# Optimization experiments

Measured on AMD Instinct MI355X. Metric: run time of the kernel, lower is better.

## Reference

```python
import jax, jax.numpy as jnp
import numpy as np

B, S, D, H = 2, 2048, 2048, 16
HD = D // H


def setup_inputs() -> dict:
    key = jax.random.key(0)
    kx, = jax.random.split(key, 1)
    return {
        "x": jax.random.normal(kx, (B, S, D), dtype=jnp.float32),
        "q_mask": jnp.ones((D, D), dtype=jnp.float32),
        "k_mask": jnp.ones((D, D), dtype=jnp.float32),
        "v_mask": jnp.ones((D, D), dtype=jnp.float32),
        "out_mask": jnp.ones((D, D), dtype=jnp.float32),
        "head_mask": jnp.ones((H,), dtype=jnp.float32),
        "attention_mask": jnp.ones((B, S), dtype=jnp.float32),
        "shared_weight": jnp.float32(1.0),
    }


def reference(x, q_mask, k_mask, v_mask, out_mask, head_mask, attention_mask, shared_weight):
    b, s, d = x.shape
    scale = jnp.float32(HD) ** -0.5

    def shared_linear(inp, mask):
        # F.linear(x, mask * shared_weight): out = inp @ (mask*sw).T
        return jnp.einsum("bsd,ed->bse", inp, mask * shared_weight)

    q = shared_linear(x, q_mask).reshape(b, s, H, HD).transpose(0, 2, 1, 3)  # [B,H,S,HD]
    k = shared_linear(x, k_mask).reshape(b, s, H, HD).transpose(0, 2, 1, 3)
    v = shared_linear(x, v_mask).reshape(b, s, H, HD).transpose(0, 2, 1, 3)

    hm = head_mask.reshape(1, H, 1, 1)
    q, k, v = q * hm, k * hm, v * hm

    scores = jnp.einsum("bhqd,bhkd->bhqk", q, k) * scale  # [B,H,S,S]

    # causal mask: upper triangle (j > i) -> -inf
    causal = jnp.triu(jnp.ones((s, s), dtype=bool), k=1)
    scores = jnp.where(causal, -jnp.inf, scores)

    # additive attention mask: (1 - m) * -10000, broadcast [B,1,1,S]
    scores = scores + (1.0 - attention_mask)[:, None, None, :] * -10000.0

    attn = jax.nn.softmax(scores, axis=-1)  # dropout is identity in eval / p=0

    out = jnp.einsum("bhqk,bhkd->bhqd", attn, v)          # [B,H,S,HD]
    out = out.transpose(0, 2, 1, 3).reshape(b, s, d)       # [B,S,D]
    return shared_linear(out, out_mask)
```

## Files before the change

### kernel.cpp

```cpp
#include <hip/hip_runtime.h>

#define B_  2
#define S_  2048
#define D_  2048
#define H_  16
#define HD_ 128

typedef __bf16 bf16;
typedef __bf16 bf16x4 __attribute__((ext_vector_type(4)));
typedef __bf16 bf16x8 __attribute__((ext_vector_type(8)));
typedef float  f32x4  __attribute__((ext_vector_type(4)));
typedef unsigned int u32x4 __attribute__((ext_vector_type(4)));

__device__ __forceinline__ void gld_lds16(const void* g, void* l) {
    __builtin_amdgcn_global_load_lds(
        (const __attribute__((address_space(1))) unsigned int*)g,
        (__attribute__((address_space(3))) unsigned int*)l, 16, 0, 0);
}

__device__ __forceinline__ f32x4 mfma16(bf16x8 a, bf16x8 b, f32x4 c) {
    return __builtin_amdgcn_mfma_f32_16x16x32_bf16(a, b, c, 0, 0, 0);
}

#define BAR()  asm volatile("s_barrier" ::: "memory")

__global__ __launch_bounds__(256)
void precast_all(const float* __restrict__ x, bf16* __restrict__ xh,
                 bf16* __restrict__ xl,
                 const float* __restrict__ qm, bf16* __restrict__ qmb,
                 const float* __restrict__ km, bf16* __restrict__ kmb,
                 const float* __restrict__ swp) {
    int bid = blockIdx.x;
    if (bid < 4096) {
        int i = (bid * 256 + threadIdx.x) * 8;
        float4 a = *(const float4*)(x + i);
        float4 b = *(const float4*)(x + i + 4);
        float av[8] = {a.x, a.y, a.z, a.w, b.x, b.y, b.z, b.w};
        bf16x8 h8, l8;
#pragma unroll
        for (int e = 0; e < 8; e++) {
            bf16 hv = (bf16)av[e];
            h8[e] = hv;
            l8[e] = (bf16)(av[e] - (float)hv);
        }
        *(bf16x8*)(xh + i) = h8;
        *(bf16x8*)(xl + i) = l8;
        return;
    }
    const float sw = swp[0];
    bid -= 4096;
    const float* src = qm; bf16* dst = qmb;
    if (bid >= 2048) { src = km; dst = kmb; bid -= 2048; }
    int i = (bid * 256 + threadIdx.x) * 8;
    float4 a = *(const float4*)(src + i);
    float4 b = *(const float4*)(src + i + 4);
    bf16x8 o;
    o[0] = (bf16)(a.x * sw); o[1] = (bf16)(a.y * sw);
    o[2] = (bf16)(a.z * sw); o[3] = (bf16)(a.w * sw);
    o[4] = (bf16)(b.x * sw); o[5] = (bf16)(b.y * sw);
    o[6] = (bf16)(b.z * sw); o[7] = (bf16)(b.w * sw);
    *(bf16x8*)(dst + i) = o;
}

__global__ __launch_bounds__(256)
void precast_mask(const float* __restrict__ s0, bf16* __restrict__ d0,
                  const float* __restrict__ swp) {
    const float sw = swp[0];
    int i = (blockIdx.x * 256 + threadIdx.x) * 8;
    float4 a = *(const float4*)(s0 + i);
    float4 b = *(const float4*)(s0 + i + 4);
    bf16x8 o;
    o[0] = (bf16)(a.x * sw); o[1] = (bf16)(a.y * sw);
    o[2] = (bf16)(a.z * sw); o[3] = (bf16)(a.w * sw);
    o[4] = (bf16)(b.x * sw); o[5] = (bf16)(b.y * sw);
    o[6] = (bf16)(b.z * sw); o[7] = (bf16)(b.w * sw);
    *(bf16x8*)(d0 + i) = o;
}

template<int BM, int BN, int MODE>
__global__ __launch_bounds__(256, 2)
void gemm2p(const bf16* __restrict__ Ah_g, const bf16* __restrict__ Al_g,
            const bf16* __restrict__ Bq, const bf16* __restrict__ Bk,
            const float* __restrict__ hm,
            bf16* __restrict__ o_qh, bf16* __restrict__ o_ql,
            bf16* __restrict__ o_kh, bf16* __restrict__ o_kl,
            bf16* __restrict__ o_vt, float* __restrict__ o_f32,
            int nt) {
    constexpr int IM = BM / 2 / 16;
    constexpr int JN = BN / 2 / 16;
    constexpr int IH = IM / 2;
    constexpr int ISSA = BM / 64;
    constexpr int ISSB = BN / 64;
    constexpr int BUFE = (BM + BN) * 32;
    constexpr int SMELEMS = (MODE == 1 && BN * (BM + 8) > 2 * BUFE)
                                ? BN * (BM + 8) : 2 * BUFE;
    __shared__ bf16 sm[SMELEMS];

    const int t = threadIdx.x;
    const int wave = t >> 6, lane = t & 63;
    const int lrow = lane & 15, quad = lane >> 4;
    const int wr = wave >> 1, wc = wave & 1;

    const int gx = gridDim.x;
    const int id0 = blockIdx.y * gx + blockIdx.x;
    const int nwg = gx * gridDim.y;
    const int id = (id0 & 7) * (nwg >> 3) + (id0 >> 3);
    const int m0 = (id / gx) * BM, n0 = (id % gx) * BN;

    const int nsec = (MODE == 0) ? (n0 & (D_ - 1)) : n0;
    const bf16* Bg = (MODE == 0 && n0 >= D_) ? Bk : Bq;

    const int arow = wr * (BM / 2) + lrow;
    const int brow = wc * (BN / 2) + lrow;
    const int gsw = (quad ^ ((lrow >> 1) & 3)) * 8;

    const int srr = lane >> 2, spg = lane & 3;
    const int ssw = (spg ^ ((srr >> 1) & 3)) * 8;

    auto stage_A = [&](int kt, int pbuf) {
        const bf16* As = (MODE == 0 && kt >= 64) ? Al_g : Ah_g;
        const int kc = ((MODE == 0) ? (kt & 63) : kt) * 32;
        bf16* buf = sm + pbuf * BUFE;
#pragma unroll
        for (int pp = 0; pp < ISSA; pp++) {
            int r0 = wave * (BM / 4) + pp * 16;
            gld_lds16(As + (size_t)(m0 + r0 + srr) * D_ + kc + ssw,
                      buf + r0 * 32);
        }
    };
    auto stage_B = [&](int kt, int pbuf) {
        const int kc = ((MODE == 0) ? (kt & 63) : kt) * 32;
        bf16* buf = sm + pbuf * BUFE + BM * 32;
#pragma unroll
        for (int pp = 0; pp < ISSB; pp++) {
            int r0 = wave * (BN / 4) + pp * 16;
            gld_lds16(Bg + (size_t)(nsec + r0 + srr) * D_ + kc + ssw,
                      buf + r0 * 32);
        }
    };

    f32x4 acc[IM][JN];
#pragma unroll
    for (int i = 0; i < IM; i++)
#pragma unroll
        for (int j = 0; j < JN; j++) acc[i][j] = (f32x4){0.f, 0.f, 0.f, 0.f};

    stage_A(0, 0); stage_B(0, 0); stage_B(1, 1);

    int p = 0;
    for (int kt = 0; kt < nt; ++kt) {
        if (kt < nt - 1) asm volatile("s_waitcnt vmcnt(2)" ::: "memory");
        else             asm volatile("s_waitcnt vmcnt(0)" ::: "memory");
        BAR();
        if (kt + 1 < nt) stage_A(kt + 1, p ^ 1);

        const bf16* Ab = sm + p * BUFE;
        const bf16* Bb = Ab + BM * 32;
        bf16x8 a[IH], b[JN];

#pragma unroll
        for (int j = 0; j < JN; j++)
            b[j] = *(const bf16x8*)&Bb[(brow + j * 16) * 32 + gsw];
#pragma unroll
        for (int i = 0; i < IH; i++)
            a[i] = *(const bf16x8*)&Ab[(arow + i * 16) * 32 + gsw];
        __builtin_amdgcn_s_setprio(1);
#pragma unroll
        for (int i = 0; i < IH; i++)
#pragma unroll
            for (int j = 0; j < JN; j++)
                acc[i][j] = mfma16(a[i], b[j], acc[i][j]);
        __builtin_amdgcn_s_setprio(0);
        BAR();

        if (kt + 2 < nt) stage_B(kt + 2, p);

#pragma unroll
        for (int i = 0; i < IH; i++)
            a[i] = *(const bf16x8*)&Ab[(arow + (IH + i) * 16) * 32 + gsw];
        __builtin_amdgcn_s_setprio(1);
#pragma unroll
        for (int i = 0; i < IH; i++)
#pragma unroll
            for (int j = 0; j < JN; j++)
                acc[IH + i][j] = mfma16(a[i], b[j], acc[IH + i][j]);
        __builtin_amdgcn_s_setprio(0);
        p ^= 1;
    }

    if constexpr (MODE == 0) {
        const bool isq = (n0 < D_);
        bf16* oh = isq ? o_qh : o_kh;
        bf16* ol = isq ? o_ql : o_kl;
#pragma unroll
        for (int j = 0; j < JN; j++) {
            int nb = nsec + wc * (BN / 2) + j * 16;
            int h = nb >> 7;
            float hv = hm[h];
#pragma unroll
            for (int i = 0; i < IM; i++) {
                int mB = m0 + wr * (BM / 2) + i * 16 + quad * 4;
                int bb = mB >> 11, s = mB & (S_ - 1);
                size_t idx0 = (((size_t)bb * H_ + h) * S_ + s) * HD_ + (nb & 127) + lrow;
#pragma unroll
                for (int r = 0; r < 4; r++) {
                    float v = acc[i][j][r] * hv;
                    bf16 hvv = (bf16)v;
                    bf16 lvv = (bf16)(v - (float)hvv);
                    oh[idx0 + (size_t)r * HD_] = hvv;
                    ol[idx0 + (size_t)r * HD_] = lvv;
                }
            }
        }
    }
    if constexpr (MODE == 1) {
        __syncthreads();
        bf16* tr = sm;
#pragma unroll
        for (int j = 0; j < JN; j++) {
            int nl = wc * (BN / 2) + j * 16 + lrow;
            float hv = hm[(n0 + nl) >> 7];
#pragma unroll
            for (int i = 0; i < IM; i++) {
                int ml = wr * (BM / 2) + i * 16 + quad * 4;
                bf16x4 pk;
#pragma unroll
                for (int r = 0; r < 4; r++) pk[r] = (bf16)(acc[i][j][r] * hv);
                *(bf16x4*)&tr[nl * 136 + ml] = pk;
            }
        }
        __syncthreads();
        const int bI = m0 >> 11;
        const int s0 = m0 & (S_ - 1);
#pragma unroll
        for (int w = 0; w < 8; w++) {
            int nrow = w * 16 + (t >> 4);
            int c = t & 15;
            bf16x8 vv = *(const bf16x8*)&tr[nrow * 136 + c * 8];
            int ng = n0 + nrow;
            int h = ng >> 7, hd = ng & 127;
            *(bf16x8*)&o_vt[((size_t)(bI * H_ + h) * HD_ + hd) * S_ + s0 + c * 8] = vv;
        }
    }
    if constexpr (MODE == 2) {
#pragma unroll
        for (int j = 0; j < JN; j++) {
            int n = n0 + wc * (BN / 2) + j * 16 + lrow;
#pragma unroll
            for (int i = 0; i < IM; i++) {
                int mB = m0 + wr * (BM / 2) + i * 16 + quad * 4;
#pragma unroll
                for (int r = 0; r < 4; r++)
                    o_f32[(size_t)(mB + r) * D_ + n] = acc[i][j][r];
            }
        }
    }
}

#define SPLD 72

__global__ __launch_bounds__(512, 2)
void attn_kernel(const bf16* __restrict__ qh_, const bf16* __restrict__ ql_,
                 const bf16* __restrict__ kh_, const bf16* __restrict__ kl_,
                 const bf16* __restrict__ vt_, const float* __restrict__ am,
                 bf16* __restrict__ outp) {
    const int id = blockIdx.x;
    const int xcd = id & 7, slot = id >> 3;
    const int bh = xcd * 4 + (slot & 3);
    const int qb = 15 - (slot >> 2);
    const int b = bh >> 4, h = bh & 15;
    const int i0 = qb * 128;
    const int t = threadIdx.x, wave = t >> 6, lane = t & 63;
    const int lrow = lane & 15, quad = lane >> 4;

    __shared__ bf16 skh[64 * 128];
    __shared__ bf16 skl[64 * 128];
    __shared__ bf16 svt[128 * 64];
    __shared__ bf16 sp[8][16 * SPLD];
    __shared__ float samadd[S_];

    const size_t kbase = (size_t)bh * S_ * HD_;
    const size_t vbase = (size_t)bh * HD_ * S_;

    {
        int j = t * 4;
        float4 a0 = *(const float4*)(am + b * S_ + j);
        float4 r0 = {(1.0f - a0.x) * -10000.0f, (1.0f - a0.y) * -10000.0f,
                     (1.0f - a0.z) * -10000.0f, (1.0f - a0.w) * -10000.0f};
        *(float4*)&samadd[j] = r0;
    }

    const int qrow = i0 + wave * 16 + lrow;
    bf16x8 qhf[4], qlf[4];
#pragma unroll
    for (int c = 0; c < 4; c++) {
        qhf[c] = *(const bf16x8*)&qh_[kbase + (size_t)qrow * HD_ + c * 32 + quad * 8];
        qlf[c] = *(const bf16x8*)&ql_[kbase + (size_t)qrow * HD_ + c * 32 + quad * 8];
    }

    u32x4 kpre[4], vpre[2];
    auto issueKV = [&](int j0) {
#pragma unroll
        for (int p = 0; p < 2; p++) {
            int rb = wave * 8 + p * 4;
            int r = rb + (lane >> 4);
            int gl = ((lane & 15) ^ (r & 7)) * 8;
            kpre[p]     = *(const u32x4*)(kh_ + kbase + (size_t)(j0 + r) * HD_ + gl);
            kpre[2 + p] = *(const u32x4*)(kl_ + kbase + (size_t)(j0 + r) * HD_ + gl);
        }
#pragma unroll
        for (int p = 0; p < 2; p++) {
            int db = wave * 16 + p * 8;
            int d = db + (lane >> 3);
            int gl = ((lane & 7) ^ (d & 7)) * 8;
            vpre[p] = *(const u32x4*)(vt_ + vbase + (size_t)d * S_ + j0 + gl);
        }
    };
    auto writeKV = [&]() {
#pragma unroll
        for (int p = 0; p < 2; p++) {
            int rb = wave * 8 + p * 4;
            *(u32x4*)&skh[rb * 128 + lane * 8] = kpre[p];
            *(u32x4*)&skl[rb * 128 + lane * 8] = kpre[2 + p];
        }
#pragma unroll
        for (int p = 0; p < 2; p++) {
            int db = wave * 16 + p * 8;
            *(u32x4*)&svt[db * 64 + lane * 8] = vpre[p];
        }
    };

    float m_i[4], l_i[4];
    f32x4 O[8];
#pragma unroll
    for (int r = 0; r < 4; r++) { m_i[r] = -INFINITY; l_i[r] = 0.f; }
#pragma unroll
    for (int n2 = 0; n2 < 8; n2++) O[n2] = (f32x4){0.f, 0.f, 0.f, 0.f};

    const float scale = 0.08838834764831845f;
    const int wbase = i0 + wave * 16;
    const int jmax = i0 + 64;

    issueKV(0);
    __syncthreads();

    for (int j0 = 0; j0 <= jmax; j0 += 64) {
        BAR();
        writeKV();
        if (j0 + 64 <= jmax) issueKV(j0 + 64);
        asm volatile("s_waitcnt lgkmcnt(0)" ::: "memory");
        BAR();

        if (j0 > wbase + 15) continue;

        float amadd[4];
#pragma unroll
        for (int nt = 0; nt < 4; nt++)
            amadd[nt] = samadd[j0 + nt * 16 + lrow];

        f32x4 s4[4];
#pragma unroll
        for (int nt = 0; nt < 4; nt++) s4[nt] = (f32x4){0.f, 0.f, 0.f, 0.f};
        __builtin_amdgcn_s_setprio(1);
#pragma unroll
        for (int c = 0; c < 4; c++) {
#pragma unroll
            for (int nt = 0; nt < 4; nt++) {
                int ka = (nt * 16 + lrow) * 128 + (((c * 4 + quad) ^ (lrow & 7)) * 8);
                bf16x8 kb8 = *(const bf16x8*)&skh[ka];
                bf16x8 lb8 = *(const bf16x8*)&skl[ka];
                s4[nt] = mfma16(qhf[c], kb8, s4[nt]);
                s4[nt] = mfma16(qhf[c], lb8, s4[nt]);
                s4[nt] = mfma16(qlf[c], kb8, s4[nt]);
            }
        }
        __builtin_amdgcn_s_setprio(0);

        const bool needmask = (j0 + 63 > wbase);
#pragma unroll
        for (int r = 0; r < 4; r++) {
            const int rglob = wbase + quad * 4 + r;
            float sv[4], pw[4];
            float mx = -INFINITY;
#pragma unroll
            for (int nt = 0; nt < 4; nt++) {
                float xv = s4[nt][r] * scale + amadd[nt];
                if (needmask && (j0 + nt * 16 + lrow) > rglob) xv = -INFINITY;
                sv[nt] = xv;
                mx = fmaxf(mx, xv);
            }
#pragma unroll
            for (int off = 1; off < 16; off <<= 1) mx = fmaxf(mx, __shfl_xor(mx, off));
            float mnew = fmaxf(m_i[r], mx);
            float alpha = __expf(m_i[r] - mnew);
            float ps = 0.f;
#pragma unroll
            for (int nt = 0; nt < 4; nt++) { pw[nt] = __expf(sv[nt] - mnew); ps += pw[nt]; }
#pragma unroll
            for (int off = 1; off < 16; off <<= 1) ps += __shfl_xor(ps, off);
            l_i[r] = l_i[r] * alpha + ps;
            m_i[r] = mnew;
#pragma unroll
            for (int n2 = 0; n2 < 8; n2++) O[n2][r] *= alpha;
#pragma unroll
            for (int nt = 0; nt < 4; nt++)
                sp[wave][(quad * 4 + r) * SPLD + nt * 16 + lrow] = (bf16)pw[nt];
        }
        asm volatile("s_waitcnt lgkmcnt(0)" ::: "memory");

        __builtin_amdgcn_s_setprio(1);
#pragma unroll
        for (int k2 = 0; k2 < 2; k2++) {
            bf16x8 pf = *(const bf16x8*)&sp[wave][lrow * SPLD + k2 * 32 + quad * 8];
            const int gp = ((quad + k2 * 4) ^ (lrow & 7)) * 8;
#pragma unroll
            for (int n2 = 0; n2 < 8; n2++) {
                bf16x8 vf8 = *(const bf16x8*)&svt[(n2 * 16 + lrow) * 64 + gp];
                O[n2] = mfma16(pf, vf8, O[n2]);
            }
        }
        __builtin_amdgcn_s_setprio(0);
    }

    float inv[4];
#pragma unroll
    for (int r = 0; r < 4; r++) inv[r] = 1.0f / l_i[r];
#pragma unroll
    for (int n2 = 0; n2 < 8; n2++)
#pragma unroll
        for (int r = 0; r < 4; r++) {
            int srow = i0 + wave * 16 + quad * 4 + r;
            outp[((size_t)(b * S_ + srow)) * D_ + h * HD_ + n2 * 16 + lrow] =
                (bf16)(O[n2][r] * inv[r]);
        }
}

extern "C" void kernel_launch(void* const* d_in, const int* in_sizes, int n_in,
                              void* d_out, int out_size, void* d_ws, size_t ws_size,
                              hipStream_t stream) {
    const float* x  = (const float*)d_in[0];
    const float* qm = (const float*)d_in[1];
    const float* km = (const float*)d_in[2];
    const float* vm = (const float*)d_in[3];
    const float* om = (const float*)d_in[4];
    const float* hm = (const float*)d_in[5];
    const float* am = (const float*)d_in[6];
    const float* sw = (const float*)d_in[7];
    float* out = (float*)d_out;

    const size_t P = (size_t)B_ * H_ * S_ * HD_ * sizeof(bf16);
    char* ws = (char*)d_ws;
    bf16* xh = (bf16*)(ws + 0 * P);
    bf16* xl = (bf16*)(ws + 1 * P);
    bf16* qh = (bf16*)(ws + 2 * P);
    bf16* ql = (bf16*)(ws + 3 * P);
    bf16* kh = (bf16*)(ws + 4 * P);
    bf16* kl = (bf16*)(ws + 5 * P);
    bf16* attn_out = xh;
    bf16* vmb = xl;
    bf16* omb = qh;
    bf16* vt  = (bf16*)d_out;
    bf16* qmb = (bf16*)((char*)d_out + 16u * 1024 * 1024);
    bf16* kmb = (bf16*)((char*)d_out + 24u * 1024 * 1024);

    precast_all<<<8192, 256, 0, stream>>>(x, xh, xl, qm, qmb, km, kmb, sw);

    gemm2p<256, 128, 0><<<dim3(32, 16), 256, 0, stream>>>(
        xh, xl, qmb, kmb, hm, qh, ql, kh, kl, nullptr, nullptr, 128);

    precast_mask<<<2048, 256, 0, stream>>>(vm, vmb, sw);
    gemm2p<128, 128, 1><<<dim3(16, 32), 256, 0, stream>>>(
        xh, nullptr, vmb, nullptr, hm,
        nullptr, nullptr, nullptr, nullptr, vt, nullptr, 64);

    attn_kernel<<<512, 512, 0, stream>>>(qh, ql, kh, kl, vt, am, attn_out);

    precast_mask<<<2048, 256, 0, stream>>>(om, omb, sw);
    gemm2p<128, 128, 2><<<dim3(16, 32), 256, 0, stream>>>(
        attn_out, nullptr, omb, nullptr, hm,
        nullptr, nullptr, nullptr, nullptr, nullptr, out, 64);
}
```

Measured before the change: 474.7 us.

## Use K=64 tiles with new swizzle for V and output projection GEMMs

Splits the single-pass GEMMs (V projection and output projection) into a dedicated kernel that stages 64-wide K slices instead of 32, halving the number of main-loop iterations and barriers. It uses a new 8-way XOR swizzle for LDS layout and issues two MFMAs per fragment pair per step. The two-pass Q/K GEMM is specialized and keeps its old 32-wide tiling. LDS use per block doubles, which may affect occupancy.

New measurement: 463.6 us. -2.3%, faster.

```diff
diff --git a/kernel.cpp b/kernel.cpp
--- a/kernel.cpp
+++ b/kernel.cpp
@@ -77,24 +77,18 @@
     *(bf16x8*)(d0 + i) = o;
 }
 
-template<int BM, int BN, int MODE>
 __global__ __launch_bounds__(256, 2)
 void gemm2p(const bf16* __restrict__ Ah_g, const bf16* __restrict__ Al_g,
             const bf16* __restrict__ Bq, const bf16* __restrict__ Bk,
             const float* __restrict__ hm,
             bf16* __restrict__ o_qh, bf16* __restrict__ o_ql,
             bf16* __restrict__ o_kh, bf16* __restrict__ o_kl,
-            bf16* __restrict__ o_vt, float* __restrict__ o_f32,
             int nt) {
-    constexpr int IM = BM / 2 / 16;
-    constexpr int JN = BN / 2 / 16;
-    constexpr int IH = IM / 2;
-    constexpr int ISSA = BM / 64;
-    constexpr int ISSB = BN / 64;
+    constexpr int BM = 256, BN = 128;
+    constexpr int IM = 8, JN = 4, IH = 4;
+    constexpr int ISSA = 4, ISSB = 2;
     constexpr int BUFE = (BM + BN) * 32;
-    constexpr int SMELEMS = (MODE == 1 && BN * (BM + 8) > 2 * BUFE)
-                                ? BN * (BM + 8) : 2 * BUFE;
-    __shared__ bf16 sm[SMELEMS];
+    __shared__ bf16 sm[2 * BUFE];
 
     const int t = threadIdx.x;
     const int wave = t >> 6, lane = t & 63;
@@ -107,8 +101,8 @@
     const int id = (id0 & 7) * (nwg >> 3) + (id0 >> 3);
     const int m0 = (id / gx) * BM, n0 = (id % gx) * BN;
 
-    const int nsec = (MODE == 0) ? (n0 & (D_ - 1)) : n0;
-    const bf16* Bg = (MODE == 0 && n0 >= D_) ? Bk : Bq;
+    const int nsec = n0 & (D_ - 1);
+    const bf16* Bg = (n0 >= D_) ? Bk : Bq;
 
     const int arow = wr * (BM / 2) + lrow;
     const int brow = wc * (BN / 2) + lrow;
@@ -118,8 +112,8 @@
     const int ssw = (spg ^ ((srr >> 1) & 3)) * 8;
 
     auto stage_A = [&](int kt, int pbuf) {
-        const bf16* As = (MODE == 0 && kt >= 64) ? Al_g : Ah_g;
-        const int kc = ((MODE == 0) ? (kt & 63) : kt) * 32;
+        const bf16* As = (kt >= 64) ? Al_g : Ah_g;
+        const int kc = (kt & 63) * 32;
         bf16* buf = sm + pbuf * BUFE;
 #pragma unroll
         for (int pp = 0; pp < ISSA; pp++) {
@@ -129,7 +123,7 @@
         }
     };
     auto stage_B = [&](int kt, int pbuf) {
-        const int kc = ((MODE == 0) ? (kt & 63) : kt) * 32;
+        const int kc = (kt & 63) * 32;
         bf16* buf = sm + pbuf * BUFE + BM * 32;
 #pragma unroll
         for (int pp = 0; pp < ISSB; pp++) {
@@ -188,41 +182,150 @@
         p ^= 1;
     }
 
-    if constexpr (MODE == 0) {
-        const bool isq = (n0 < D_);
-        bf16* oh = isq ? o_qh : o_kh;
-        bf16* ol = isq ? o_ql : o_kl;
+    const bool isq = (n0 < D_);
+    bf16* oh = isq ? o_qh : o_kh;
+    bf16* ol = isq ? o_ql : o_kl;
+#pragma unroll
+    for (int j = 0; j < JN; j++) {
+        int nb = nsec + wc * (BN / 2) + j * 16;
+        int h = nb >> 7;
+        float hv = hm[h];
+#pragma unroll
+        for (int i = 0; i < IM; i++) {
+            int mB = m0 + wr * (BM / 2) + i * 16 + quad * 4;
+            int bb = mB >> 11, s = mB & (S_ - 1);
+            size_t idx0 = (((size_t)bb * H_ + h) * S_ + s) * HD_ + (nb & 127) + lrow;
+#pragma unroll
+            for (int r = 0; r < 4; r++) {
+                float v = acc[i][j][r] * hv;
+                bf16 hvv = (bf16)v;
+                bf16 lvv = (bf16)(v - (float)hvv);
+                oh[idx0 + (size_t)r * HD_] = hvv;
+                ol[idx0 + (size_t)r * HD_] = lvv;
+            }
+        }
+    }
+}
+
+template<int MODE>
+__global__ __launch_bounds__(256, 2)
+void gemm64(const bf16* __restrict__ A_g, const bf16* __restrict__ B_g,
+            const float* __restrict__ hm,
+            bf16* __restrict__ o_vt, float* __restrict__ o_f32, int nt) {
+    constexpr int BM = 128, BN = 128;
+    constexpr int IM = 4, JN = 4, IH = 2;
+    constexpr int BUFE = (BM + BN) * 64;
+    __shared__ bf16 sm[2 * BUFE];
+
+    const int t = threadIdx.x;
+    const int wave = t >> 6, lane = t & 63;
+    const int lrow = lane & 15, quad = lane >> 4;
+    const int wr = wave >> 1, wc = wave & 1;
+
+    const int gx = gridDim.x;
+    const int id0 = blockIdx.y * gx + blockIdx.x;
+    const int nwg = gx * gridDim.y;
+    const int id = (id0 & 7) * (nwg >> 3) + (id0 >> 3);
+    const int m0 = (id / gx) * BM, n0 = (id % gx) * BN;
+
+    const int arow = wr * 64 + lrow;
+    const int brow = wc * 64 + lrow;
+    const int g0e = (quad ^ (lrow & 7)) * 8;
+    const int g1e = ((quad + 4) ^ (lrow & 7)) * 8;
+
+    const int srr8 = lane >> 3, sgp = lane & 7;
+    const int ssw = (sgp ^ srr8) * 8;
+
+    auto stage_A = [&](int kt, int pbuf) {
+        const int kc = kt * 64;
+        bf16* buf = sm + pbuf * BUFE;
+#pragma unroll
+        for (int pp = 0; pp < 4; pp++) {
+            int r0 = wave * 32 + pp * 8;
+            gld_lds16(A_g + (size_t)(m0 + r0 + srr8) * D_ + kc + ssw,
+                      buf + r0 * 64);
+        }
+    };
+    auto stage_B = [&](int kt, int pbuf) {
+        const int kc = kt * 64;
+        bf16* buf = sm + pbuf * BUFE + BM * 64;
+#pragma unroll
+        for (int pp = 0; pp < 4; pp++) {
+            int r0 = wave * 32 + pp * 8;
+            gld_lds16(B_g + (size_t)(n0 + r0 + srr8) * D_ + kc + ssw,
+                      buf + r0 * 64);
+        }
+    };
+
+    f32x4 acc[IM][JN];
+#pragma unroll
+    for (int i = 0; i < IM; i++)
+#pragma unroll
+        for (int j = 0; j < JN; j++) acc[i][j] = (f32x4){0.f, 0.f, 0.f, 0.f};
+
+    stage_A(0, 0); stage_B(0, 0); stage_B(1, 1);
+
+    int p = 0;
+    for (int kt = 0; kt < nt; ++kt) {
+        if (kt < nt - 1) asm volatile("s_waitcnt vmcnt(4)" ::: "memory");
+        else             asm volatile("s_waitcnt vmcnt(0)" ::: "memory");
+        BAR();
+        if (kt + 1 < nt) stage_A(kt + 1, p ^ 1);
+
+        const bf16* Ab = sm + p * BUFE;
+        const bf16* Bb = Ab + BM * 64;
+        bf16x8 b0[JN], b1[JN], a0[IH], a1[IH];
+
 #pragma unroll
         for (int j = 0; j < JN; j++) {
-            int nb = nsec + wc * (BN / 2) + j * 16;
-            int h = nb >> 7;
-            float hv = hm[h];
-#pragma unroll
-            for (int i = 0; i < IM; i++) {
-                int mB = m0 + wr * (BM / 2) + i * 16 + quad * 4;
-                int bb = mB >> 11, s = mB & (S_ - 1);
-                size_t idx0 = (((size_t)bb * H_ + h) * S_ + s) * HD_ + (nb & 127) + lrow;
-#pragma unroll
-                for (int r = 0; r < 4; r++) {
-                    float v = acc[i][j][r] * hv;
-                    bf16 hvv = (bf16)v;
-                    bf16 lvv = (bf16)(v - (float)hvv);
-                    oh[idx0 + (size_t)r * HD_] = hvv;
-                    ol[idx0 + (size_t)r * HD_] = lvv;
-                }
-            }
-        }
-    }
+            b0[j] = *(const bf16x8*)&Bb[(brow + j * 16) * 64 + g0e];
+            b1[j] = *(const bf16x8*)&Bb[(brow + j * 16) * 64 + g1e];
+        }
+#pragma unroll
+        for (int i = 0; i < IH; i++) {
+            a0[i] = *(const bf16x8*)&Ab[(arow + i * 16) * 64 + g0e];
+            a1[i] = *(const bf16x8*)&Ab[(arow + i * 16) * 64 + g1e];
+        }
+        __builtin_amdgcn_s_setprio(1);
+#pragma unroll
+        for (int i = 0; i < IH; i++)
+#pragma unroll
+            for (int j = 0; j < JN; j++) {
+                acc[i][j] = mfma16(a0[i], b0[j], acc[i][j]);
+                acc[i][j] = mfma16(a1[i], b1[j], acc[i][j]);
+            }
+        __builtin_amdgcn_s_setprio(0);
+        BAR();
+
+        if (kt + 2 < nt) stage_B(kt + 2, p);
+
+#pragma unroll
+        for (int i = 0; i < IH; i++) {
+            a0[i] = *(const bf16x8*)&Ab[(arow + (IH + i) * 16) * 64 + g0e];
+            a1[i] = *(const bf16x8*)&Ab[(arow + (IH + i) * 16) * 64 + g1e];
+        }
+        __builtin_amdgcn_s_setprio(1);
+#pragma unroll
+        for (int i = 0; i < IH; i++)
+#pragma unroll
+            for (int j = 0; j < JN; j++) {
+                acc[IH + i][j] = mfma16(a0[i], b0[j], acc[IH + i][j]);
+                acc[IH + i][j] = mfma16(a1[i], b1[j], acc[IH + i][j]);
+            }
+        __builtin_amdgcn_s_setprio(0);
+        p ^= 1;
+    }
+
     if constexpr (MODE == 1) {
         __syncthreads();
         bf16* tr = sm;
 #pragma unroll
         for (int j = 0; j < JN; j++) {
-            int nl = wc * (BN / 2) + j * 16 + lrow;
+            int nl = wc * 64 + j * 16 + lrow;
             float hv = hm[(n0 + nl) >> 7];
 #pragma unroll
             for (int i = 0; i < IM; i++) {
-                int ml = wr * (BM / 2) + i * 16 + quad * 4;
+                int ml = wr * 64 + i * 16 + quad * 4;
                 bf16x4 pk;
 #pragma unroll
                 for (int r = 0; r < 4; r++) pk[r] = (bf16)(acc[i][j][r] * hv);
@@ -245,10 +348,10 @@
     if constexpr (MODE == 2) {
 #pragma unroll
         for (int j = 0; j < JN; j++) {
-            int n = n0 + wc * (BN / 2) + j * 16 + lrow;
+            int n = n0 + wc * 64 + j * 16 + lrow;
 #pragma unroll
             for (int i = 0; i < IM; i++) {
-                int mB = m0 + wr * (BM / 2) + i * 16 + quad * 4;
+                int mB = m0 + wr * 64 + i * 16 + quad * 4;
 #pragma unroll
                 for (int r = 0; r < 4; r++)
                     o_f32[(size_t)(mB + r) * D_ + n] = acc[i][j][r];
@@ -465,18 +568,16 @@
 
     precast_all<<<8192, 256, 0, stream>>>(x, xh, xl, qm, qmb, km, kmb, sw);
 
-    gemm2p<256, 128, 0><<<dim3(32, 16), 256, 0, stream>>>(
-        xh, xl, qmb, kmb, hm, qh, ql, kh, kl, nullptr, nullptr, 128);
+    gemm2p<<<dim3(32, 16), 256, 0, stream>>>(
+        xh, xl, qmb, kmb, hm, qh, ql, kh, kl, 128);
 
     precast_mask<<<2048, 256, 0, stream>>>(vm, vmb, sw);
-    gemm2p<128, 128, 1><<<dim3(16, 32), 256, 0, stream>>>(
-        xh, nullptr, vmb, nullptr, hm,
-        nullptr, nullptr, nullptr, nullptr, vt, nullptr, 64);
+    gemm64<1><<<dim3(16, 32), 256, 0, stream>>>(
+        xh, vmb, hm, vt, nullptr, 32);
 
     attn_kernel<<<512, 512, 0, stream>>>(qh, ql, kh, kl, vt, am, attn_out);
 
     precast_mask<<<2048, 256, 0, stream>>>(om, omb, sw);
-    gemm2p<128, 128, 2><<<dim3(16, 32), 256, 0, stream>>>(
-        attn_out, nullptr, omb, nullptr, hm,
-        nullptr, nullptr, nullptr, nullptr, nullptr, out, 64);
-}
+    gemm64<2><<<dim3(16, 32), 256, 0, stream>>>(
+        attn_out, omb, hm, nullptr, out, 32);
+}
```
